# Optimization experiments

Hardware: AMD Instinct MI355X
Metric: run time of the kernel (lower is better)

## Reference

```python
import math
import jax, jax.numpy as jnp
import numpy as np

B, T, H, A, F = 2, 2048, 2048, 2048, 8192
L, LID, EPS = 24, 0, 1e-5
NEG_INF = -1e38


def setup_inputs() -> dict:
    key = jax.random.key(0)
    ks = jax.random.split(key, 8)
    s = 0.02
    # RWKV init-derived time parameters for layer_id=0, num_hidden_layers=24
    ratio_0_to_1 = LID / (L - 1)          # 0.0
    ratio_1_to_almost_0 = 1.0 - LID / L    # 1.0
    x = jnp.arange(H, dtype=jnp.float32) / H
    tmk = jnp.power(x, ratio_1_to_almost_0)
    tmv = tmk + 0.3 * ratio_0_to_1
    tmr = jnp.power(x, 0.5 * ratio_1_to_almost_0)
    zigzag = 0.5 * (jnp.arange(1, A + 1, dtype=jnp.float32) % 3 - 1)
    time_first = jnp.full((A,), math.log(0.3), dtype=jnp.float32) + zigzag
    h = jnp.arange(A, dtype=jnp.float32)
    time_decay = -5.0 + 8.0 * (h / (A - 1)) ** (0.7 + 1.3 * ratio_0_to_1)
    return {
        'hidden': jax.random.normal(ks[0], (B, T, H), jnp.float32),
        'pre_w': jnp.ones((H,), jnp.float32), 'pre_b': jnp.zeros((H,), jnp.float32),
        'ln1_w': jnp.ones((H,), jnp.float32), 'ln1_b': jnp.zeros((H,), jnp.float32),
        'ln2_w': jnp.ones((H,), jnp.float32), 'ln2_b': jnp.zeros((H,), jnp.float32),
        'time_decay': time_decay, 'time_first': time_first,
        'tmk': tmk, 'tmv': tmv, 'tmr': tmr,
        'Wk': jax.random.normal(ks[1], (H, A), jnp.float32) * s,
        'Wv': jax.random.normal(ks[2], (H, A), jnp.float32) * s,
        'Wr': jax.random.normal(ks[3], (H, A), jnp.float32) * s,
        'Wo': jax.random.normal(ks[4], (A, H), jnp.float32) * s,
        'f_tmk': jnp.power(x, ratio_1_to_almost_0), 'f_tmr': jnp.power(x, ratio_1_to_almost_0),
        'f_Wk': jax.random.normal(ks[5], (H, F), jnp.float32) * s,
        'f_Wr': jax.random.normal(ks[6], (H, H), jnp.float32) * s,
        'f_Wv': jax.random.normal(ks[7], (F, H), jnp.float32) * s,
    }


def _ln(x, w, b):
    mu = x.mean(-1, keepdims=True)
    var = ((x - mu) ** 2).mean(-1, keepdims=True)
    return (x - mu) * jax.lax.rsqrt(var + EPS) * w + b


def _token_shift(x):
    # sx state is zeros at init: prepend a zero row, drop the last token
    return jnp.concatenate((jnp.zeros_like(x[:, :1, :]), x[:, :-1, :]), axis=1)


def _forward(hidden, pre_w, pre_b, ln1_w, ln1_b, ln2_w, ln2_b,
             time_decay, time_first, tmk, tmv, tmr, Wk, Wv, Wr, Wo,
             f_tmk, f_tmr, f_Wk, f_Wr, f_Wv):
    h0 = _ln(hidden, pre_w, pre_b)          # pre_ln (layer_id == 0)
    # ---- time mixing (RwkvSelfAttention) ----
    x1 = _ln(h0, ln1_w, ln1_b)
    cx = _token_shift(x1)
    kx = x1 * tmk + cx * (1 - tmk)
    vx = x1 * tmv + cx * (1 - tmv)
    rx = x1 * tmr + cx * (1 - tmr)
    r = jax.nn.sigmoid(rx @ Wr)             # [B,T,A]
    k = kx @ Wk
    v = vx @ Wv
    w_decay = -jnp.exp(time_decay)          # [A]

    def step(carry, kv):
        aa, bb, pp = carry                  # each [B,A]
        kk, vv = kv                         # each [B,A]
        ww = time_first + kk
        q = jnp.maximum(pp, ww)
        e1 = jnp.exp(pp - q)
        e2 = jnp.exp(ww - q)
        out = (e1 * aa + e2 * vv) / (e1 * bb + e2)
        ww2 = w_decay + pp
        q2 = jnp.maximum(ww2, kk)
        e1 = jnp.exp(ww2 - q2)
        e2 = jnp.exp(kk - q2)
        return (e1 * aa + e2 * vv, e1 * bb + e2, q2), out

    init = (jnp.zeros((B, A), k.dtype), jnp.zeros((B, A), k.dtype),
            jnp.full((B, A), NEG_INF, jnp.float32))
    _, wkv = jax.lax.scan(step, init, (jnp.swapaxes(k, 0, 1), jnp.swapaxes(v, 0, 1)))
    wkv = jnp.swapaxes(wkv, 0, 1)           # [B,T,A]
    h1 = h0 + (r * wkv) @ Wo
    # ---- channel mixing (RwkvFeedForward) ----
    x2 = _ln(h1, ln2_w, ln2_b)
    cx2 = _token_shift(x2)
    kx2 = x2 * f_tmk + cx2 * (1 - f_tmk)
    rx2 = x2 * f_tmr + cx2 * (1 - f_tmr)
    r2 = jax.nn.sigmoid(rx2 @ f_Wr)
    kk2 = jnp.square(jax.nn.relu(kx2 @ f_Wk))
    return h1 + r2 * (kk2 @ f_Wv)


def reference(hidden, pre_w, pre_b, ln1_w, ln1_b, ln2_w, ln2_b,
              time_decay, time_first, tmk, tmv, tmr, Wk, Wv, Wr, Wo,
              f_tmk, f_tmr, f_Wk, f_Wr, f_Wv):
    return _forward(hidden, pre_w, pre_b, ln1_w, ln1_b, ln2_w, ln2_b,
                    time_decay, time_first, tmk, tmv, tmr, Wk, Wv, Wr, Wo,
                    f_tmk, f_tmr, f_Wk, f_Wr, f_Wv)
```

## Files before the change

### kernel.cpp

```cpp
#include <hip/hip_runtime.h>

#define B_  2
#define T_  2048
#define H_  2048
#define A_  2048
#define F_  8192
#define BT_ 4096

typedef __bf16  bf16x8 __attribute__((ext_vector_type(8)));
typedef float   f32x4  __attribute__((ext_vector_type(4)));
typedef short   short8 __attribute__((ext_vector_type(8)));

__device__ __forceinline__ float bf2f(unsigned short b) {
  return __uint_as_float(((unsigned)b) << 16);
}
__device__ __forceinline__ unsigned short f2bf(float f) {
  unsigned u = __float_as_uint(f);
  unsigned r = (u + 0x7FFFu + ((u >> 16) & 1u)) >> 16;
  return (unsigned short)r;
}

typedef __attribute__((address_space(3))) void lds_void_t;
typedef __attribute__((address_space(1))) const void gc_void_t;
__device__ __forceinline__ void gload_lds16(const void* g, void* l) {
  __builtin_amdgcn_global_load_lds((gc_void_t*)g, (lds_void_t*)l, 16, 0, 0);
}

__global__ void canary_kernel(float* out) { out[threadIdx.x] = 1000.0f; }

__global__ __launch_bounds__(256) void transpose_bf16_kernel(
    const float* __restrict__ src, unsigned short* __restrict__ dst, int Kd, int Nd)
{
  __shared__ float tile[32][33];
  const int tx = threadIdx.x & 31;
  const int ty = threadIdx.x >> 5;
  const int n0 = blockIdx.x * 32;
  const int k0 = blockIdx.y * 32;
#pragma unroll
  for (int i = 0; i < 32; i += 8)
    tile[ty + i][tx] = src[(size_t)(k0 + ty + i) * Nd + n0 + tx];
  __syncthreads();
#pragma unroll
  for (int i = 0; i < 32; i += 8)
    dst[(size_t)(n0 + ty + i) * Kd + k0 + tx] = f2bf(tile[tx][ty + i]);
}

__device__ __forceinline__ void block_reduce2(float& a, float& b) {
#pragma unroll
  for (int off = 32; off > 0; off >>= 1) {
    a += __shfl_down(a, off, 64);
    b += __shfl_down(b, off, 64);
  }
  __shared__ float sa[4], sb[4];
  const int lane = threadIdx.x & 63, w = threadIdx.x >> 6;
  __syncthreads();
  if (lane == 0) { sa[w] = a; sb[w] = b; }
  __syncthreads();
  a = sa[0] + sa[1] + sa[2] + sa[3];
  b = sb[0] + sb[1] + sb[2] + sb[3];
}

__global__ __launch_bounds__(256) void ln_pre_kernel(
    const float* __restrict__ hidden,
    const float* __restrict__ pw, const float* __restrict__ pb,
    const float* __restrict__ w1, const float* __restrict__ b1,
    float* __restrict__ h0, unsigned short* __restrict__ x1)
{
  const int row = blockIdx.x, tid = threadIdx.x;
  const int c0 = tid * 8;
  const size_t base = (size_t)row * H_ + c0;
  float x[8];
  float4 v0 = *(const float4*)(hidden + base);
  float4 v1 = *(const float4*)(hidden + base + 4);
  x[0]=v0.x; x[1]=v0.y; x[2]=v0.z; x[3]=v0.w;
  x[4]=v1.x; x[5]=v1.y; x[6]=v1.z; x[7]=v1.w;
  float s = 0.f, s2 = 0.f;
#pragma unroll
  for (int j = 0; j < 8; ++j) { s += x[j]; s2 += x[j]*x[j]; }
  block_reduce2(s, s2);
  float mu  = s * (1.f / H_);
  float inv = rsqrtf(fmaxf(s2 * (1.f / H_) - mu*mu, 0.f) + 1e-5f);
  float y[8];
#pragma unroll
  for (int j = 0; j < 8; ++j) y[j] = (x[j] - mu) * inv * pw[c0+j] + pb[c0+j];
  *(float4*)(h0 + base)     = make_float4(y[0],y[1],y[2],y[3]);
  *(float4*)(h0 + base + 4) = make_float4(y[4],y[5],y[6],y[7]);
  s = 0.f; s2 = 0.f;
#pragma unroll
  for (int j = 0; j < 8; ++j) { s += y[j]; s2 += y[j]*y[j]; }
  block_reduce2(s, s2);
  mu  = s * (1.f / H_);
  inv = rsqrtf(fmaxf(s2 * (1.f / H_) - mu*mu, 0.f) + 1e-5f);
  unsigned o[4];
#pragma unroll
  for (int p = 0; p < 4; ++p) {
    unsigned lo = f2bf((y[2*p]   - mu) * inv * w1[c0+2*p]   + b1[c0+2*p]);
    unsigned hi = f2bf((y[2*p+1] - mu) * inv * w1[c0+2*p+1] + b1[c0+2*p+1]);
    o[p] = lo | (hi << 16);
  }
  *(uint4*)(x1 + base) = make_uint4(o[0], o[1], o[2], o[3]);
}

__global__ __launch_bounds__(256) void ln_single_kernel(
    const float* __restrict__ in, const float* __restrict__ w_, const float* __restrict__ b_,
    unsigned short* __restrict__ outb)
{
  const int row = blockIdx.x, tid = threadIdx.x;
  const int c0 = tid * 8;
  const size_t base = (size_t)row * H_ + c0;
  float x[8];
  float4 v0 = *(const float4*)(in + base);
  float4 v1 = *(const float4*)(in + base + 4);
  x[0]=v0.x; x[1]=v0.y; x[2]=v0.z; x[3]=v0.w;
  x[4]=v1.x; x[5]=v1.y; x[6]=v1.z; x[7]=v1.w;
  float s = 0.f, s2 = 0.f;
#pragma unroll
  for (int j = 0; j < 8; ++j) { s += x[j]; s2 += x[j]*x[j]; }
  block_reduce2(s, s2);
  float mu  = s * (1.f / H_);
  float inv = rsqrtf(fmaxf(s2 * (1.f / H_) - mu*mu, 0.f) + 1e-5f);
  unsigned o[4];
#pragma unroll
  for (int p = 0; p < 4; ++p) {
    unsigned lo = f2bf((x[2*p]   - mu) * inv * w_[c0+2*p]   + b_[c0+2*p]);
    unsigned hi = f2bf((x[2*p+1] - mu) * inv * w_[c0+2*p+1] + b_[c0+2*p+1]);
    o[p] = lo | (hi << 16);
  }
  *(uint4*)(outb + base) = make_uint4(o[0], o[1], o[2], o[3]);
}

__global__ __launch_bounds__(256) void mix1_kernel(
    const unsigned short* __restrict__ x,
    const float* __restrict__ tm_,
    unsigned short* __restrict__ outb)
{
  const int row = blockIdx.x;
  const int t = row & (T_ - 1);
  const int c0 = threadIdx.x * 8;
  const size_t base = (size_t)row * H_ + c0;
  uint4 xv = *(const uint4*)(x + base);
  uint4 cv = make_uint4(0u,0u,0u,0u);
  if (t > 0) cv = *(const uint4*)(x + base - H_);
  const unsigned xs[4] = {xv.x, xv.y, xv.z, xv.w};
  const unsigned cs[4] = {cv.x, cv.y, cv.z, cv.w};
  unsigned oo[4];
#pragma unroll
  for (int p = 0; p < 4; ++p) {
    unsigned w = 0;
#pragma unroll
    for (int h = 0; h < 2; ++h) {
      const int j = p*2 + h;
      float xf = bf2f((unsigned short)((xs[p] >> (h*16)) & 0xFFFFu));
      float cf = bf2f((unsigned short)((cs[p] >> (h*16)) & 0xFFFFu));
      w |= (unsigned)f2bf(fmaf(xf - cf, tm_[c0+j], cf)) << (h*16);
    }
    oo[p] = w;
  }
  *(uint4*)(outb + base) = make_uint4(oo[0],oo[1],oo[2],oo[3]);
}

#define WKV_G 32
#define WKV_C 32
#define WKV_L 64

__global__ __launch_bounds__(1024) void wkv_scan_kernel(
    const unsigned short* __restrict__ kg, const unsigned short* __restrict__ vg,
    const unsigned short* __restrict__ rg,
    const float* __restrict__ time_first, const float* __restrict__ time_decay,
    unsigned short* __restrict__ rwkv)
{
  const int tid = threadIdx.x;
  const int al  = tid & (WKV_G - 1);
  const int c   = tid >> 5;
  const int b   = blockIdx.x >> 6;
  const int ag  = blockIdx.x & 63;
  const int a   = ag * WKV_G + al;
  const float tf = time_first[a];
  const float w  = -__expf(time_decay[a]);
  const size_t cb = (size_t)b * T_ * A_ + a + (size_t)c * WKV_L * A_;

  float aa = 0.f, bb = 0.f, pp = -1e38f;
  {
    float kb[4], vb[4];
#pragma unroll
    for (int j = 0; j < 4; ++j) {
      kb[j] = bf2f(kg[cb + (size_t)j * A_]);
      vb[j] = bf2f(vg[cb + (size_t)j * A_]);
    }
    for (int t0 = 0; t0 < WKV_L; t0 += 4) {
#pragma unroll
      for (int j = 0; j < 4; ++j) {
        const float kk = kb[j], vv = vb[j];
        const int tn = t0 + j + 4;
        if (tn < WKV_L) {
          kb[j] = bf2f(kg[cb + (size_t)tn * A_]);
          vb[j] = bf2f(vg[cb + (size_t)tn * A_]);
        }
        float ww2 = w + pp;
        float q2  = fmaxf(ww2, kk);
        float e1  = __expf(ww2 - q2);
        float e2  = __expf(kk  - q2);
        aa = e1*aa + e2*vv;
        bb = e1*bb + e2;
        pp = q2;
      }
    }
  }
  __shared__ float saa[WKV_C][WKV_G], sbb[WKV_C][WKV_G], spp[WKV_C][WKV_G];
  saa[c][al] = aa; sbb[c][al] = bb; spp[c][al] = pp;
  __syncthreads();

  if (tid < WKV_G) {
    float Aa = 0.f, Bb = 0.f, Pp = -1e38f;
    const float Lw = (float)WKV_L * w;
    for (int cc = 0; cc < WKV_C; ++cc) {
      const float na = saa[cc][tid], nb = sbb[cc][tid], np = spp[cc][tid];
      saa[cc][tid] = Aa; sbb[cc][tid] = Bb; spp[cc][tid] = Pp;
      const float p1 = Pp + Lw;
      const float pc = fmaxf(p1, np);
      const float f1 = __expf(p1 - pc);
      const float f2 = __expf(np - pc);
      Aa = f1*Aa + f2*na;
      Bb = f1*Bb + f2*nb;
      Pp = pc;
    }
  }
  __syncthreads();
  aa = saa[c][al]; bb = sbb[c][al]; pp = spp[c][al];

  {
    float kb[4], vb[4], rb[4];
#pragma unroll
    for (int j = 0; j < 4; ++j) {
      kb[j] = bf2f(kg[cb + (size_t)j * A_]);
      vb[j] = bf2f(vg[cb + (size_t)j * A_]);
      rb[j] = bf2f(rg[cb + (size_t)j * A_]);
    }
    for (int t0 = 0; t0 < WKV_L; t0 += 4) {
#pragma unroll
      for (int j = 0; j < 4; ++j) {
        const float kk = kb[j], vv = vb[j], rr = rb[j];
        const int tn = t0 + j + 4;
        if (tn < WKV_L) {
          kb[j] = bf2f(kg[cb + (size_t)tn * A_]);
          vb[j] = bf2f(vg[cb + (size_t)tn * A_]);
          rb[j] = bf2f(rg[cb + (size_t)tn * A_]);
        }
        float ww = tf + kk;
        float q  = fmaxf(pp, ww);
        float e1 = __expf(pp - q);
        float e2 = __expf(ww - q);
        float o  = (e1*aa + e2*vv) / (e1*bb + e2);
        float sr = 1.f / (1.f + __expf(-rr));
        rwkv[cb + (size_t)(t0 + j) * A_] = f2bf(sr * o);
        float ww2 = w + pp;
        float q2  = fmaxf(ww2, kk);
        e1 = __expf(ww2 - q2);
        e2 = __expf(kk  - q2);
        aa = e1*aa + e2*vv;
        bb = e1*bb + e2;
        pp = q2;
      }
    }
  }
}

enum { EPI_BF16 = 0, EPI_ADDIP = 1, EPI_RELU2 = 2, EPI_SIGADD = 3 };

template <int RG, int CG, int EPI>
__global__ __launch_bounds__(512) void gemm4_kernel(
    const unsigned short* __restrict__ Ap, const unsigned short* __restrict__ Bp,
    void* __restrict__ Cp, int K, int Nn,
    const unsigned short* __restrict__ sigb)
{
  constexpr int BM = 128, BN = 256;
  constexpr int FM = 4, FN = 4;
  __shared__ unsigned short As[3 * BM * 64];
  __shared__ unsigned short Bs[3 * BN * 64];
  const int tid  = threadIdx.x;
  const int lane = tid & 63;
  const int lr = lane & 15;
  const int hi = lane >> 4;
  const int rx7 = lr & 7;
  const int wid = tid >> 6;
  const int wm = wid >> 2, wn = wid & 3;
  const int rowW = wm * 64;
  const int colW = wn * 64;
  const int gx = gridDim.x;
  const int gy = gridDim.y;
  const int flat = blockIdx.y * gx + blockIdx.x;
  const int xcd = flat & 7;
  const int j = flat >> 3;
  const int rgc = gy / RG;
  const int r_idx = xcd % rgc;
  const int c_idx = xcd / rgc;
  const int row_l = j % RG;
  const int col_l = j / RG;
  const long row0 = (long)(r_idx * RG + row_l) * BM;
  const long col0 = (long)(c_idx * CG + col_l) * BN;
  const unsigned short* Ab = Ap + (size_t)row0 * K;
  const unsigned short* Bb = Bp + (size_t)col0 * K;
  const int srow8 = tid >> 3;
  const int sslot = (tid & 7) ^ (srow8 & 7);
  f32x4 acc[FM][FN] = {};

#define SP0(bufi, tt) do {                                                        \
    unsigned short* asb = As + (bufi) * (BM * 64);                                \
    unsigned short* bsb = Bs + (bufi) * (BN * 64);                                \
    const size_t ko = (size_t)(tt) * 64 + sslot * 8;                              \
    gload_lds16(Ab + (size_t)srow8        * K + ko, asb + tid * 8);               \
    gload_lds16(Ab + (size_t)(srow8 + 64) * K + ko, asb + 4096 + tid * 8);        \
    gload_lds16(Bb + (size_t)srow8        * K + ko, bsb + tid * 8);               \
  } while (0)
#define SP1(bufi, tt) do {                                                        \
    unsigned short* bsb = Bs + (bufi) * (BN * 64);                                \
    const size_t ko = (size_t)(tt) * 64 + sslot * 8;                              \
    gload_lds16(Bb + (size_t)(srow8 + 64)  * K + ko, bsb + 4096  + tid * 8);      \
    gload_lds16(Bb + (size_t)(srow8 + 128) * K + ko, bsb + 8192  + tid * 8);      \
    gload_lds16(Bb + (size_t)(srow8 + 192) * K + ko, bsb + 12288 + tid * 8);      \
  } while (0)

  const int nt = K >> 6;
  SP0(0, 0); SP1(0, 0);
  SP0(1, 1); SP1(1, 1);
  int cur = 0;
  for (int t = 0; t < nt; ++t) {
    if (t + 1 < nt) asm volatile("s_waitcnt vmcnt(6)" ::: "memory");
    else            asm volatile("s_waitcnt vmcnt(0)" ::: "memory");
    __builtin_amdgcn_s_barrier();
    int nb = cur + 2; if (nb >= 3) nb -= 3;
    const unsigned short* asb = As + cur * (BM * 64);
    const unsigned short* bsb = Bs + cur * (BN * 64);
#pragma unroll
    for (int kk = 0; kk < 2; ++kk) {
      bf16x8 af[FM], bfr[FN];
#pragma unroll
      for (int m = 0; m < FM; ++m) {
        const int row = rowW + m*16 + lr;
        const int ps = (kk*4 + hi) ^ rx7;
        af[m] = __builtin_bit_cast(bf16x8, *(const short8*)(asb + row*64 + ps*8));
      }
#pragma unroll
      for (int n = 0; n < FN; ++n) {
        const int row = colW + n*16 + lr;
        const int ps = (kk*4 + hi) ^ rx7;
        bfr[n] = __builtin_bit_cast(bf16x8, *(const short8*)(bsb + row*64 + ps*8));
      }
      if (t + 2 < nt) { if (kk == 0) SP0(nb, t + 2); else SP1(nb, t + 2); }
      asm volatile("s_waitcnt lgkmcnt(0)" ::: "memory");
      __builtin_amdgcn_sched_barrier(0);
      __builtin_amdgcn_s_setprio(1);
#pragma unroll
      for (int m = 0; m < FM; ++m)
#pragma unroll
        for (int n = 0; n < FN; ++n)
          acc[m][n] = __builtin_amdgcn_mfma_f32_16x16x32_bf16(af[m], bfr[n], acc[m][n], 0, 0, 0);
      __builtin_amdgcn_s_setprio(0);
      if (kk == 0) __builtin_amdgcn_s_barrier();
    }
    cur = (cur + 1 == 3) ? 0 : cur + 1;
  }
#undef SP0
#undef SP1

#pragma unroll
  for (int m = 0; m < FM; ++m) {
#pragma unroll
    for (int n = 0; n < FN; ++n) {
      const long col = col0 + colW + n*16 + lr;
#pragma unroll
      for (int j2 = 0; j2 < 4; ++j2) {
        const long row = row0 + rowW + m*16 + hi*4 + j2;
        const size_t idx = (size_t)row * Nn + col;
        const float v = acc[m][n][j2];
        if (EPI == EPI_BF16) {
          ((unsigned short*)Cp)[idx] = f2bf(v);
        } else if (EPI == EPI_ADDIP) {
          float* C = (float*)Cp;
          C[idx] = C[idx] + v;
        } else if (EPI == EPI_RELU2) {
          float rr = v > 0.f ? v : 0.f;
          ((unsigned short*)Cp)[idx] = f2bf(rr * rr);
        } else {
          float s = 1.f / (1.f + __expf(-bf2f(sigb[idx])));
          float* C = (float*)Cp;
          C[idx] = C[idx] + s * v;
        }
      }
    }
  }
}

#define MB(x) ((size_t)(x) << 20)
#define WS_NEED MB(184)

extern "C" void kernel_launch(void* const* d_in, const int* in_sizes, int n_in,
                              void* d_out, int out_size, void* d_ws, size_t ws_size,
                              hipStream_t stream) {
  const float* hidden     = (const float*)d_in[0];
  const float* pre_w      = (const float*)d_in[1];
  const float* pre_b      = (const float*)d_in[2];
  const float* ln1_w      = (const float*)d_in[3];
  const float* ln1_b      = (const float*)d_in[4];
  const float* ln2_w      = (const float*)d_in[5];
  const float* ln2_b      = (const float*)d_in[6];
  const float* time_decay = (const float*)d_in[7];
  const float* time_first = (const float*)d_in[8];
  const float* tmk        = (const float*)d_in[9];
  const float* tmv        = (const float*)d_in[10];
  const float* tmr        = (const float*)d_in[11];
  const float* Wk         = (const float*)d_in[12];
  const float* Wv         = (const float*)d_in[13];
  const float* Wr         = (const float*)d_in[14];
  const float* Wo         = (const float*)d_in[15];
  const float* f_tmk      = (const float*)d_in[16];
  const float* f_tmr      = (const float*)d_in[17];
  const float* f_Wk       = (const float*)d_in[18];
  const float* f_Wr       = (const float*)d_in[19];
  const float* f_Wv       = (const float*)d_in[20];
  float* out = (float*)d_out;
  char*  ws  = (char*)d_ws;

  if (ws_size < WS_NEED) {
    canary_kernel<<<1, 256, 0, stream>>>(out);
    return;
  }

  unsigned short* fWkT = (unsigned short*)(ws + MB(0));
  unsigned short* fWvT = (unsigned short*)(ws + MB(32));
  unsigned short* WkT  = (unsigned short*)(ws + MB(64));
  unsigned short* WvT  = (unsigned short*)(ws + MB(72));
  unsigned short* WrT  = (unsigned short*)(ws + MB(80));
  unsigned short* WoT  = (unsigned short*)(ws + MB(88));
  unsigned short* fWrT = (unsigned short*)(ws + MB(96));
  unsigned short* KK   = (unsigned short*)(ws + MB(64));
  unsigned short* S1   = (unsigned short*)(ws + MB(104));
  unsigned short* S4   = (unsigned short*)(ws + MB(120));
  unsigned short* S2   = (unsigned short*)(ws + MB(136));
  unsigned short* S3   = (unsigned short*)(ws + MB(152));
  unsigned short* M1   = (unsigned short*)(ws + MB(168));

  const dim3 blk(256);
  const dim3 blk512(512);
  const dim3 gSmall(8, 32);
  const dim3 gRelu(32, 32);


  transpose_bf16_kernel<<<dim3(64, 64),  blk, 0, stream>>>(Wk,   WkT,  2048, 2048);
  transpose_bf16_kernel<<<dim3(64, 64),  blk, 0, stream>>>(Wv,   WvT,  2048, 2048);
  transpose_bf16_kernel<<<dim3(64, 64),  blk, 0, stream>>>(Wr,   WrT,  2048, 2048);
  transpose_bf16_kernel<<<dim3(64, 64),  blk, 0, stream>>>(Wo,   WoT,  2048, 2048);
  transpose_bf16_kernel<<<dim3(64, 64),  blk, 0, stream>>>(f_Wr, fWrT, 2048, 2048);
  transpose_bf16_kernel<<<dim3(256, 64), blk, 0, stream>>>(f_Wk, fWkT, 2048, 8192);
  transpose_bf16_kernel<<<dim3(64, 256), blk, 0, stream>>>(f_Wv, fWvT, 8192, 2048);

  ln_pre_kernel<<<BT_, blk, 0, stream>>>(hidden, pre_w, pre_b, ln1_w, ln1_b, out, S1);

  mix1_kernel<<<BT_, blk, 0, stream>>>(S1, tmk, M1);
  gemm4_kernel<8,4,EPI_BF16><<<gSmall, blk512, 0, stream>>>(M1, WkT, S2, 2048, 2048, nullptr);
  mix1_kernel<<<BT_, blk, 0, stream>>>(S1, tmv, M1);
  gemm4_kernel<8,4,EPI_BF16><<<gSmall, blk512, 0, stream>>>(M1, WvT, S3, 2048, 2048, nullptr);
  mix1_kernel<<<BT_, blk, 0, stream>>>(S1, tmr, M1);
  gemm4_kernel<8,4,EPI_BF16><<<gSmall, blk512, 0, stream>>>(M1, WrT, S4, 2048, 2048, nullptr);

  wkv_scan_kernel<<<dim3(128), dim3(1024), 0, stream>>>(S2, S3, S4, time_first, time_decay, S1);

  gemm4_kernel<8,4,EPI_ADDIP><<<gSmall, blk512, 0, stream>>>(S1, WoT, out, 2048, 2048, nullptr);

  ln_single_kernel<<<BT_, blk, 0, stream>>>(out, ln2_w, ln2_b, S2);

  mix1_kernel<<<BT_, blk, 0, stream>>>(S2, f_tmr, M1);
  gemm4_kernel<8,4,EPI_BF16><<<gSmall, blk512, 0, stream>>>(M1, fWrT, S3, 2048, 2048, nullptr);

  mix1_kernel<<<BT_, blk, 0, stream>>>(S2, f_tmk, M1);

  gemm4_kernel<8,16,EPI_RELU2><<<gRelu, blk512, 0, stream>>>(M1, fWkT, KK, 2048, 8192, nullptr);
  gemm4_kernel<8,4,EPI_SIGADD><<<gSmall, blk512, 0, stream>>>(KK, fWvT, out, 8192, 2048, S3);
}
```

Before: 740.7 us.

## Fuse LN2 with channel-mix token shift; use 256x256 double-buffered tile for FFN key GEMM

Replaces the separate ln_single plus two mix1 launches for channel mixing with one kernel. It recomputes layernorm for both the current and the previous row and writes the kx2 and rx2 bf16 inputs directly, removing two launches and the intermediate round trip. The gemm kernel is templated on the M tile and buffer count, and the large 4096x8192 relu-squared GEMM now uses a 256x256 tile with two LDS buffers instead of three, so each B tile is reused across more rows. The costs are recomputing the layernorm statistics for the previous row, and a shallower prefetch pipeline with larger register and LDS use in the big GEMM.

```diff
diff --git a/kernel.cpp b/kernel.cpp
--- a/kernel.cpp
+++ b/kernel.cpp
@@ -101,32 +101,61 @@
   *(uint4*)(x1 + base) = make_uint4(o[0], o[1], o[2], o[3]);
 }
 
-__global__ __launch_bounds__(256) void ln_single_kernel(
-    const float* __restrict__ in, const float* __restrict__ w_, const float* __restrict__ b_,
-    unsigned short* __restrict__ outb)
+__global__ __launch_bounds__(256) void lnmix2_kernel(
+    const float* __restrict__ h1,
+    const float* __restrict__ w_, const float* __restrict__ b_,
+    const float* __restrict__ tmk_, const float* __restrict__ tmr_,
+    unsigned short* __restrict__ kx2b, unsigned short* __restrict__ rx2b)
 {
   const int row = blockIdx.x, tid = threadIdx.x;
+  const int t = row & (T_ - 1);
   const int c0 = tid * 8;
   const size_t base = (size_t)row * H_ + c0;
-  float x[8];
-  float4 v0 = *(const float4*)(in + base);
-  float4 v1 = *(const float4*)(in + base + 4);
-  x[0]=v0.x; x[1]=v0.y; x[2]=v0.z; x[3]=v0.w;
-  x[4]=v1.x; x[5]=v1.y; x[6]=v1.z; x[7]=v1.w;
+  float x[8], p[8];
+  {
+    float4 v0 = *(const float4*)(h1 + base);
+    float4 v1 = *(const float4*)(h1 + base + 4);
+    x[0]=v0.x; x[1]=v0.y; x[2]=v0.z; x[3]=v0.w;
+    x[4]=v1.x; x[5]=v1.y; x[6]=v1.z; x[7]=v1.w;
+  }
+  const bool hasp = (t > 0);
+  if (hasp) {
+    float4 v0 = *(const float4*)(h1 + base - H_);
+    float4 v1 = *(const float4*)(h1 + base - H_ + 4);
+    p[0]=v0.x; p[1]=v0.y; p[2]=v0.z; p[3]=v0.w;
+    p[4]=v1.x; p[5]=v1.y; p[6]=v1.z; p[7]=v1.w;
+  } else {
+#pragma unroll
+    for (int j = 0; j < 8; ++j) p[j] = 0.f;
+  }
   float s = 0.f, s2 = 0.f;
 #pragma unroll
   for (int j = 0; j < 8; ++j) { s += x[j]; s2 += x[j]*x[j]; }
   block_reduce2(s, s2);
-  float mu  = s * (1.f / H_);
-  float inv = rsqrtf(fmaxf(s2 * (1.f / H_) - mu*mu, 0.f) + 1e-5f);
-  unsigned o[4];
-#pragma unroll
-  for (int p = 0; p < 4; ++p) {
-    unsigned lo = f2bf((x[2*p]   - mu) * inv * w_[c0+2*p]   + b_[c0+2*p]);
-    unsigned hi = f2bf((x[2*p+1] - mu) * inv * w_[c0+2*p+1] + b_[c0+2*p+1]);
-    o[p] = lo | (hi << 16);
-  }
-  *(uint4*)(outb + base) = make_uint4(o[0], o[1], o[2], o[3]);
+  const float mu  = s * (1.f / H_);
+  const float inv = rsqrtf(fmaxf(s2 * (1.f / H_) - mu*mu, 0.f) + 1e-5f);
+  float sp = 0.f, sp2 = 0.f;
+#pragma unroll
+  for (int j = 0; j < 8; ++j) { sp += p[j]; sp2 += p[j]*p[j]; }
+  block_reduce2(sp, sp2);
+  const float mup  = sp * (1.f / H_);
+  const float invp = rsqrtf(fmaxf(sp2 * (1.f / H_) - mup*mup, 0.f) + 1e-5f);
+  unsigned ok[4], orr[4];
+#pragma unroll
+  for (int q = 0; q < 4; ++q) {
+    unsigned ko = 0, ro = 0;
+#pragma unroll
+    for (int h = 0; h < 2; ++h) {
+      const int j = q*2 + h;
+      const float xr = (x[j] - mu) * inv * w_[c0+j] + b_[c0+j];
+      const float cr = hasp ? (p[j] - mup) * invp * w_[c0+j] + b_[c0+j] : 0.f;
+      ko |= (unsigned)f2bf(fmaf(xr - cr, tmk_[c0+j], cr)) << (h*16);
+      ro |= (unsigned)f2bf(fmaf(xr - cr, tmr_[c0+j], cr)) << (h*16);
+    }
+    ok[q] = ko; orr[q] = ro;
+  }
+  *(uint4*)(kx2b + base) = make_uint4(ok[0],ok[1],ok[2],ok[3]);
+  *(uint4*)(rx2b + base) = make_uint4(orr[0],orr[1],orr[2],orr[3]);
 }
 
 __global__ __launch_bounds__(256) void mix1_kernel(
@@ -267,16 +296,17 @@
 
 enum { EPI_BF16 = 0, EPI_ADDIP = 1, EPI_RELU2 = 2, EPI_SIGADD = 3 };
 
-template <int RG, int CG, int EPI>
+template <int BM, int NBUF, int RG, int CG, int EPI>
 __global__ __launch_bounds__(512) void gemm4_kernel(
     const unsigned short* __restrict__ Ap, const unsigned short* __restrict__ Bp,
     void* __restrict__ Cp, int K, int Nn,
     const unsigned short* __restrict__ sigb)
 {
-  constexpr int BM = 128, BN = 256;
-  constexpr int FM = 4, FN = 4;
-  __shared__ unsigned short As[3 * BM * 64];
-  __shared__ unsigned short Bs[3 * BN * 64];
+  constexpr int BN = 256;
+  constexpr int FM = BM / 32;
+  constexpr int FN = 4;
+  __shared__ unsigned short As[NBUF * BM * 64];
+  __shared__ unsigned short Bs[NBUF * BN * 64];
   const int tid  = threadIdx.x;
   const int lane = tid & 63;
   const int lr = lane & 15;
@@ -284,7 +314,7 @@
   const int rx7 = lr & 7;
   const int wid = tid >> 6;
   const int wm = wid >> 2, wn = wid & 3;
-  const int rowW = wm * 64;
+  const int rowW = wm * (BM / 2);
   const int colW = wn * 64;
   const int gx = gridDim.x;
   const int gy = gridDim.y;
@@ -304,31 +334,49 @@
   const int sslot = (tid & 7) ^ (srow8 & 7);
   f32x4 acc[FM][FN] = {};
 
-#define SP0(bufi, tt) do {                                                        \
-    unsigned short* asb = As + (bufi) * (BM * 64);                                \
-    unsigned short* bsb = Bs + (bufi) * (BN * 64);                                \
-    const size_t ko = (size_t)(tt) * 64 + sslot * 8;                              \
-    gload_lds16(Ab + (size_t)srow8        * K + ko, asb + tid * 8);               \
-    gload_lds16(Ab + (size_t)(srow8 + 64) * K + ko, asb + 4096 + tid * 8);        \
-    gload_lds16(Bb + (size_t)srow8        * K + ko, bsb + tid * 8);               \
-  } while (0)
-#define SP1(bufi, tt) do {                                                        \
-    unsigned short* bsb = Bs + (bufi) * (BN * 64);                                \
-    const size_t ko = (size_t)(tt) * 64 + sslot * 8;                              \
-    gload_lds16(Bb + (size_t)(srow8 + 64)  * K + ko, bsb + 4096  + tid * 8);      \
-    gload_lds16(Bb + (size_t)(srow8 + 128) * K + ko, bsb + 8192  + tid * 8);      \
-    gload_lds16(Bb + (size_t)(srow8 + 192) * K + ko, bsb + 12288 + tid * 8);      \
-  } while (0)
+  auto SP0 = [&](int bufi, int tt) {
+    unsigned short* asb = As + bufi * (BM * 64);
+    unsigned short* bsb = Bs + bufi * (BN * 64);
+    const size_t ko = (size_t)tt * 64 + sslot * 8;
+    if constexpr (BM == 128) {
+      gload_lds16(Ab + (size_t)srow8        * K + ko, asb + tid * 8);
+      gload_lds16(Ab + (size_t)(srow8 + 64) * K + ko, asb + 4096 + tid * 8);
+      gload_lds16(Bb + (size_t)srow8        * K + ko, bsb + tid * 8);
+    } else {
+      gload_lds16(Ab + (size_t)srow8         * K + ko, asb + tid * 8);
+      gload_lds16(Ab + (size_t)(srow8 + 64)  * K + ko, asb + 4096  + tid * 8);
+      gload_lds16(Ab + (size_t)(srow8 + 128) * K + ko, asb + 8192  + tid * 8);
+      gload_lds16(Ab + (size_t)(srow8 + 192) * K + ko, asb + 12288 + tid * 8);
+    }
+  };
+  auto SP1 = [&](int bufi, int tt) {
+    unsigned short* bsb = Bs + bufi * (BN * 64);
+    const size_t ko = (size_t)tt * 64 + sslot * 8;
+    if constexpr (BM == 128) {
+      gload_lds16(Bb + (size_t)(srow8 + 64)  * K + ko, bsb + 4096  + tid * 8);
+      gload_lds16(Bb + (size_t)(srow8 + 128) * K + ko, bsb + 8192  + tid * 8);
+      gload_lds16(Bb + (size_t)(srow8 + 192) * K + ko, bsb + 12288 + tid * 8);
+    } else {
+      gload_lds16(Bb + (size_t)srow8         * K + ko, bsb + tid * 8);
+      gload_lds16(Bb + (size_t)(srow8 + 64)  * K + ko, bsb + 4096  + tid * 8);
+      gload_lds16(Bb + (size_t)(srow8 + 128) * K + ko, bsb + 8192  + tid * 8);
+      gload_lds16(Bb + (size_t)(srow8 + 192) * K + ko, bsb + 12288 + tid * 8);
+    }
+  };
 
   const int nt = K >> 6;
   SP0(0, 0); SP1(0, 0);
-  SP0(1, 1); SP1(1, 1);
+  if constexpr (NBUF == 3) { SP0(1, 1); SP1(1, 1); }
   int cur = 0;
   for (int t = 0; t < nt; ++t) {
-    if (t + 1 < nt) asm volatile("s_waitcnt vmcnt(6)" ::: "memory");
-    else            asm volatile("s_waitcnt vmcnt(0)" ::: "memory");
+    if constexpr (NBUF == 3) {
+      if (t + 1 < nt) asm volatile("s_waitcnt vmcnt(6)" ::: "memory");
+      else            asm volatile("s_waitcnt vmcnt(0)" ::: "memory");
+    } else {
+      asm volatile("s_waitcnt vmcnt(0)" ::: "memory");
+    }
     __builtin_amdgcn_s_barrier();
-    int nb = cur + 2; if (nb >= 3) nb -= 3;
+    int nb = cur + (NBUF - 1); if (nb >= NBUF) nb -= NBUF;
     const unsigned short* asb = As + cur * (BM * 64);
     const unsigned short* bsb = Bs + cur * (BN * 64);
 #pragma unroll
@@ -346,7 +394,7 @@
         const int ps = (kk*4 + hi) ^ rx7;
         bfr[n] = __builtin_bit_cast(bf16x8, *(const short8*)(bsb + row*64 + ps*8));
       }
-      if (t + 2 < nt) { if (kk == 0) SP0(nb, t + 2); else SP1(nb, t + 2); }
+      if (t + NBUF - 1 < nt) { if (kk == 0) SP0(nb, t + NBUF - 1); else SP1(nb, t + NBUF - 1); }
       asm volatile("s_waitcnt lgkmcnt(0)" ::: "memory");
       __builtin_amdgcn_sched_barrier(0);
       __builtin_amdgcn_s_setprio(1);
@@ -358,10 +406,8 @@
       __builtin_amdgcn_s_setprio(0);
       if (kk == 0) __builtin_amdgcn_s_barrier();
     }
-    cur = (cur + 1 == 3) ? 0 : cur + 1;
-  }
-#undef SP0
-#undef SP1
+    cur = (cur + 1 == NBUF) ? 0 : cur + 1;
+  }
 
 #pragma unroll
   for (int m = 0; m < FM; ++m) {
@@ -443,8 +489,7 @@
   const dim3 blk(256);
   const dim3 blk512(512);
   const dim3 gSmall(8, 32);
-  const dim3 gRelu(32, 32);
-
+  const dim3 gRelu(32, 16);
 
   transpose_bf16_kernel<<<dim3(64, 64),  blk, 0, stream>>>(Wk,   WkT,  2048, 2048);
   transpose_bf16_kernel<<<dim3(64, 64),  blk, 0, stream>>>(Wv,   WvT,  2048, 2048);
@@ -457,23 +502,21 @@
   ln_pre_kernel<<<BT_, blk, 0, stream>>>(hidden, pre_w, pre_b, ln1_w, ln1_b, out, S1);
 
   mix1_kernel<<<BT_, blk, 0, stream>>>(S1, tmk, M1);
-  gemm4_kernel<8,4,EPI_BF16><<<gSmall, blk512, 0, stream>>>(M1, WkT, S2, 2048, 2048, nullptr);
+  gemm4_kernel<128,3,8,4,EPI_BF16><<<gSmall, blk512, 0, stream>>>(M1, WkT, S2, 2048, 2048, nullptr);
   mix1_kernel<<<BT_, blk, 0, stream>>>(S1, tmv, M1);
-  gemm4_kernel<8,4,EPI_BF16><<<gSmall, blk512, 0, stream>>>(M1, WvT, S3, 2048, 2048, nullptr);
+  gemm4_kernel<128,3,8,4,EPI_BF16><<<gSmall, blk512, 0, stream>>>(M1, WvT, S3, 2048, 2048, nullptr);
   mix1_kernel<<<BT_, blk, 0, stream>>>(S1, tmr, M1);
-  gemm4_kernel<8,4,EPI_BF16><<<gSmall, blk512, 0, stream>>>(M1, WrT, S4, 2048, 2048, nullptr);
+  gemm4_kernel<128,3,8,4,EPI_BF16><<<gSmall, blk512, 0, stream>>>(M1, WrT, S4, 2048, 2048, nullptr);
 
   wkv_scan_kernel<<<dim3(128), dim3(1024), 0, stream>>>(S2, S3, S4, time_first, time_decay, S1);
 
-  gemm4_kernel<8,4,EPI_ADDIP><<<gSmall, blk512, 0, stream>>>(S1, WoT, out, 2048, 2048, nullptr);
-
-  ln_single_kernel<<<BT_, blk, 0, stream>>>(out, ln2_w, ln2_b, S2);
-
-  mix1_kernel<<<BT_, blk, 0, stream>>>(S2, f_tmr, M1);
-  gemm4_kernel<8,4,EPI_BF16><<<gSmall, blk512, 0, stream>>>(M1, fWrT, S3, 2048, 2048, nullptr);
-
-  mix1_kernel<<<BT_, blk, 0, stream>>>(S2, f_tmk, M1);
-
-  gemm4_kernel<8,16,EPI_RELU2><<<gRelu, blk512, 0, stream>>>(M1, fWkT, KK, 2048, 8192, nullptr);
-  gemm4_kernel<8,4,EPI_SIGADD><<<gSmall, blk512, 0, stream>>>(KK, fWvT, out, 8192, 2048, S3);
-}
+  gemm4_kernel<128,3,8,4,EPI_ADDIP><<<gSmall, blk512, 0, stream>>>(S1, WoT, out, 2048, 2048, nullptr);
+
+  lnmix2_kernel<<<BT_, blk, 0, stream>>>(out, ln2_w, ln2_b, f_tmk, f_tmr, M1, S2);
+
+  gemm4_kernel<128,3,8,4,EPI_BF16><<<gSmall, blk512, 0, stream>>>(S2, fWrT, S3, 2048, 2048, nullptr);
+
+  gemm4_kernel<256,2,8,8,EPI_RELU2><<<gRelu, blk512, 0, stream>>>(M1, fWkT, KK, 2048, 8192, nullptr);
+
+  gemm4_kernel<128,3,8,4,EPI_SIGADD><<<gSmall, blk512, 0, stream>>>(KK, fWvT, out, 8192, 2048, S3);
+}
```

Result: faster. 708.6 us (-4.3%).
